# Performance work log

Measured on AMD Instinct MI355X. Metric: run time of the kernel, lower is better.

The kernel has to match this reference:

```python
import jax, jax.numpy as jnp
import numpy as np

N, E, H = 1024, 2048, 32
DIMS = [4, 128, 512, 1028]
NEG_SLOPE_ATT = 0.2   # GATv2 attention LeakyReLU
NEG_SLOPE_ACT = 0.01  # torch.nn.LeakyReLU default


def _lin(key, fan_in, fan_out):
    k1, k2 = jax.random.split(key)
    s = 1.0 / np.sqrt(fan_in)
    return (jax.random.uniform(k1, (fan_in, fan_out), jnp.float32, -s, s),
            jax.random.uniform(k2, (fan_out,), jnp.float32, -s, s))


def setup_inputs() -> dict:
    key = jax.random.key(0)
    ks = jax.random.split(key, 32)
    inp = {
        'x': jax.random.normal(ks[0], (N, 4), jnp.float32),
        'edge_index': jax.random.randint(ks[1], (2, E), 0, N, jnp.int64),
    }
    # GATv2 layers: lin_l/lin_r -> heads*out, att [H, C], bias [C]
    ki = 2
    for i in range(3):
        cin, cout = DIMS[i], DIMS[i + 1]
        wl, bl = _lin(ks[ki], cin, H * cout); ki += 1
        wr, br = _lin(ks[ki], cin, H * cout); ki += 1
        att = jax.random.normal(ks[ki], (H, cout), jnp.float32) * 0.05; ki += 1
        bias = jnp.zeros((cout,), jnp.float32)
        j = i + 1
        inp.update({f'w{j}l': wl, f'b{j}l': bl, f'w{j}r': wr, f'b{j}r': br,
                    f'att{j}': att, f'gb{j}': bias})
    # decoder MLP 1028 -> 512 -> 128 -> 2
    for j, (cin, cout) in enumerate([(1028, 512), (512, 128), (128, 2)], 1):
        w, b = _lin(ks[ki], cin, cout); ki += 1
        inp[f'dw{j}'] = w
        inp[f'db{j}'] = b
    return inp


def _gatv2(x, src, dst, wl, bl, wr, br, att, bias, cout):
    # lin_l on source nodes, lin_r on target nodes (PyG GATv2Conv)
    xl = (x @ wl + bl).reshape(-1, H, cout)   # [N, H, C]
    xr = (x @ wr + br).reshape(-1, H, cout)
    e = jax.nn.leaky_relu(xl[src] + xr[dst], NEG_SLOPE_ATT)  # [Etot, H, C]
    score = jnp.einsum('ehc,hc->eh', e, att)                  # [Etot, H]
    smax = jax.ops.segment_max(score, dst, num_segments=N)
    alpha = jnp.exp(score - smax[dst])
    denom = jax.ops.segment_sum(alpha, dst, num_segments=N)
    alpha = alpha / denom[dst]
    out = jax.ops.segment_sum(alpha[:, :, None] * xl[src], dst, num_segments=N)
    return out.mean(axis=1) + bias  # concat=False: average heads


def reference(x, edge_index,
              w1l, b1l, w1r, b1r, att1, gb1,
              w2l, b2l, w2r, b2r, att2, gb2,
              w3l, b3l, w3r, b3r, att3, gb3,
              dw1, db1, dw2, db2, dw3, db3):
    # add self loops (PyG default)
    loop = jnp.arange(N, dtype=edge_index.dtype)
    src = jnp.concatenate([edge_index[0], loop])
    dst = jnp.concatenate([edge_index[1], loop])

    act = lambda z: jax.nn.leaky_relu(z, NEG_SLOPE_ACT)
    z = _gatv2(x, src, dst, w1l, b1l, w1r, b1r, att1, gb1, 128)
    z = act(z)
    z = _gatv2(z, src, dst, w2l, b2l, w2r, b2r, att2, gb2, 512)
    z = act(z)
    z = _gatv2(z, src, dst, w3l, b3l, w3r, b3r, att3, gb3, 1028)

    z = act(z @ dw1 + db1)
    z = act(z @ dw2 + db2)
    z = z @ dw3 + db3  # [N, 2]
    return z.reshape(-1)
```

## Files before the change

kernel.cpp:

```cpp
#include <hip/hip_runtime.h>
#include <cstdint>
#include <cstddef>

#define NN 1024
#define EE 2048
#define ETOT 3072
#define HH 32

typedef __bf16 bf16_t;
typedef __attribute__((ext_vector_type(8))) __bf16 bf16x8;
typedef __attribute__((ext_vector_type(4))) __bf16 bf16x4;
typedef __attribute__((ext_vector_type(2))) __bf16 bf16x2;
typedef __attribute__((ext_vector_type(4))) float f32x4;

typedef const __attribute__((address_space(1))) void gvoid_t;
typedef __attribute__((address_space(3))) void lvoid_t;

__device__ __forceinline__ void gll16(const void* g, void* l) {
    __builtin_amdgcn_global_load_lds((gvoid_t*)g, (lvoid_t*)l, 16, 0, 0);
}

__global__ void k_zero_int(int* p, int n) {
    int i = blockIdx.x * 256 + threadIdx.x;
    if (i < n) p[i] = 0;
}

__global__ void k_detect(const int* ei, int* flag) {
    int i = blockIdx.x * 256 + threadIdx.x;
    int idx = 2 * i + 1;
    if (idx < 2 * EE && ei[idx] != 0) atomicOr(flag, 1);
}

__global__ void k_edge_prep(const int* ei, const int* flag, int* srcA, int* dstA, int* cnt) {
    int e = blockIdx.x * 256 + threadIdx.x;
    if (e >= ETOT) return;
    int s, d;
    if (e < EE) {
        if (*flag) { s = ei[e]; d = ei[EE + e]; }
        else       { s = ei[2 * e]; d = ei[2 * (EE + e)]; }
        s &= (NN - 1); d &= (NN - 1);
    } else {
        s = d = e - EE;
    }
    srcA[e] = s; dstA[e] = d;
    atomicAdd(&cnt[d], 1);
}

__global__ void k_scan(const int* cnt, int* off) {
    __shared__ int sh[NN];
    int t = threadIdx.x;
    sh[t] = cnt[t];
    __syncthreads();
    for (int o = 1; o < NN; o <<= 1) {
        int v = (t >= o) ? sh[t - o] : 0;
        __syncthreads();
        sh[t] += v;
        __syncthreads();
    }
    off[t + 1] = sh[t];
    if (t == 0) off[0] = 0;
}

__global__ void k_fill(const int* dstA, const int* off, int* cur, int* csre) {
    int e = blockIdx.x * 256 + threadIdx.x;
    if (e >= ETOT) return;
    int d = dstA[e];
    int p = atomicAdd(&cur[d], 1);
    csre[off[d] + p] = e;
}

__global__ void k_convA(const float* __restrict__ A, bf16_t* __restrict__ Ab,
                        int M, int K, int Kp) {
    int idx = blockIdx.x * 256 + threadIdx.x;
    if (idx >= M * Kp) return;
    int m = idx / Kp, k = idx % Kp;
    Ab[idx] = (k < K) ? (bf16_t)A[(size_t)m * K + k] : (bf16_t)0.f;
}

__global__ void k_convB(const float* __restrict__ B, bf16_t* __restrict__ Bt,
                        int K, int Nsub, int ldb, int Kp) {
    __shared__ float sh[32][33];
    int kt = blockIdx.y * 32, nt = blockIdx.x * 32;
    int tx = threadIdx.x & 31, ty = threadIdx.x >> 5;
#pragma unroll
    for (int i = 0; i < 4; ++i) {
        int k = kt + ty + i * 8, n = nt + tx;
        sh[ty + i * 8][tx] = (k < K && n < Nsub) ? B[(size_t)k * ldb + n] : 0.f;
    }
    __syncthreads();
    int kq = (threadIdx.x & 7) * 4;
    int nl = threadIdx.x >> 3;
    int n = nt + nl;
    if (n < Nsub) {
        bf16x4 v;
        v[0] = (bf16_t)sh[kq][nl];
        v[1] = (bf16_t)sh[kq + 1][nl];
        v[2] = (bf16_t)sh[kq + 2][nl];
        v[3] = (bf16_t)sh[kq + 3][nl];
        *(bf16x4*)(&Bt[(size_t)n * Kp + kt + kq]) = v;
    }
}

__global__ __launch_bounds__(256) void k_gemm_bf16(
        const bf16_t* __restrict__ Ab, const bf16_t* __restrict__ Bt,
        const float* __restrict__ bias, void* __restrict__ Cm,
        int M, int Nsub, int Kp, int act, int obf) {
    __shared__ __align__(16) bf16_t SH[24576];
    int tid = threadIdx.x;
    int wave = tid >> 6, lane = tid & 63;
    int wm = (wave & 1) * 64, wn = (wave >> 1) * 64;
    int l16 = lane & 15, lq = lane >> 4;

    int nx = gridDim.x, ny = gridDim.y;
    int bx = blockIdx.x, by = blockIdx.y;
    int total = nx * ny;
    if ((total & 7) == 0) {
        int j = bx + nx * by;
        int w = (j & 7) * (total >> 3) + (j >> 3);
        bx = w / ny;
        by = w % ny;
    }
    int m0 = by * 128, n0 = bx * 128;

    int u0 = wave * 128 + lane;
    int u1 = u0 + 64;
    int r0 = u0 >> 2, s0 = u0 & 3;
    int r1 = u1 >> 2, s1 = u1 & 3;
    int c0 = ((s0 ^ ((r0 >> 1) & 3)) << 3);
    int c1 = ((s1 ^ ((r1 >> 1) & 3)) << 3);
    const bf16_t* gA0 = Ab + (size_t)(m0 + r0) * Kp + c0;
    const bf16_t* gA1 = Ab + (size_t)(m0 + r1) * Kp + c1;
    const bf16_t* gB0 = Bt + (size_t)(n0 + r0) * Kp + c0;
    const bf16_t* gB1 = Bt + (size_t)(n0 + r1) * Kp + c1;

    int cR = ((lq ^ ((l16 >> 1) & 3)) << 3);

    f32x4 acc[4][4] = {};
    int nt = Kp >> 5;

#pragma unroll
    for (int pt = 0; pt < 2; ++pt) {
        bf16_t* d = SH + pt * 8192 + wave * 1024;
        gll16(gA0, d); gll16(gA1, d + 512);
        gll16(gB0, d + 4096); gll16(gB1, d + 4096 + 512);
        gA0 += 32; gA1 += 32; gB0 += 32; gB1 += 32;
    }

    int bc = 0, bn = 2;
    for (int t = 0; t < nt; ++t) {
        if (t + 1 < nt)
            asm volatile("s_waitcnt vmcnt(4) lgkmcnt(0)" ::: "memory");
        else
            asm volatile("s_waitcnt vmcnt(0) lgkmcnt(0)" ::: "memory");
        asm volatile("s_barrier" ::: "memory");
        __builtin_amdgcn_sched_barrier(0);
        if (t + 2 < nt) {
            bf16_t* d = SH + bn * 8192 + wave * 1024;
            gll16(gA0, d); gll16(gA1, d + 512);
            gll16(gB0, d + 4096); gll16(gB1, d + 4096 + 512);
            gA0 += 32; gA1 += 32; gB0 += 32; gB1 += 32;
        }
        const bf16_t* rb = SH + bc * 8192;
        bf16x8 af[4], bfr[4];
#pragma unroll
        for (int mi = 0; mi < 4; ++mi)
            af[mi] = *(const bf16x8*)(rb + (wm + mi * 16 + l16) * 32 + cR);
#pragma unroll
        for (int ni = 0; ni < 4; ++ni)
            bfr[ni] = *(const bf16x8*)(rb + 4096 + (wn + ni * 16 + l16) * 32 + cR);
#pragma unroll
        for (int mi = 0; mi < 4; ++mi)
#pragma unroll
            for (int ni = 0; ni < 4; ++ni)
                acc[mi][ni] = __builtin_amdgcn_mfma_f32_16x16x32_bf16(
                    af[mi], bfr[ni], acc[mi][ni], 0, 0, 0);
        bc = (bc == 2) ? 0 : bc + 1;
        bn = (bn == 2) ? 0 : bn + 1;
    }
    asm volatile("s_waitcnt lgkmcnt(0)" ::: "memory");
    asm volatile("s_barrier" ::: "memory");
    __builtin_amdgcn_sched_barrier(0);

    if (obf) {
#pragma unroll
        for (int ni = 0; ni < 4; ++ni) {
            int cl = wn + ni * 16 + l16;
            float bv = bias[n0 + cl];
#pragma unroll
            for (int mi = 0; mi < 4; ++mi)
#pragma unroll
                for (int r = 0; r < 4; ++r) {
                    int rl = wm + mi * 16 + lq * 4 + r;
                    float v = acc[mi][ni][r] + bv;
                    if (act && v < 0.f) v *= 0.01f;
                    int slot = ((cl >> 3) ^ (rl & 7)) & 15;
                    SH[rl * 128 + slot * 8 + (cl & 7)] = (bf16_t)v;
                }
        }
        __syncthreads();
        bf16_t* Cb = (bf16_t*)Cm;
#pragma unroll
        for (int i = 0; i < 8; ++i) {
            int j = i * 2048 + tid * 8;
            int rl = j >> 7;
            int p = (j >> 3) & 15;
            int cl = ((p ^ (rl & 7)) & 15) * 8;
            bf16x8 v = *(const bf16x8*)(SH + rl * 128 + p * 8);
            int row = m0 + rl, col = n0 + cl;
            if (row < M) {
                if (col + 7 < Nsub) {
                    *(bf16x8*)(Cb + (size_t)row * Nsub + col) = v;
                } else {
#pragma unroll
                    for (int e = 0; e < 8; ++e)
                        if (col + e < Nsub) Cb[(size_t)row * Nsub + col + e] = v[e];
                }
            }
        }
    } else {
#pragma unroll
        for (int ni = 0; ni < 4; ++ni) {
            int col = n0 + wn + ni * 16 + l16;
            if (col >= Nsub) continue;
            float bv = bias[col];
#pragma unroll
            for (int mi = 0; mi < 4; ++mi)
#pragma unroll
                for (int r = 0; r < 4; ++r) {
                    int row = m0 + wm + mi * 16 + lq * 4 + r;
                    if (row < M) {
                        float v = acc[mi][ni][r] + bv;
                        if (act && v < 0.f) v *= 0.01f;
                        ((float*)Cm)[(size_t)row * Nsub + col] = v;
                    }
                }
        }
    }
}

#define TM 64
#define TN 64
#define TK 16
__global__ __launch_bounds__(256) void k_gemm(
        const float* __restrict__ A, const float* __restrict__ B,
        const float* __restrict__ bias, void* __restrict__ Cm,
        int M, int Nsub, int K, int ldb, int act, int obf) {
    __shared__ float As[TK][TM];
    __shared__ float Bs[TK][TN];
    int tid = threadIdx.x;
    int tx = tid % 16, ty = tid / 16;
    int m0 = blockIdx.y * TM, n0 = blockIdx.x * TN;
    float acc[4][4] = {};
    for (int k0 = 0; k0 < K; k0 += TK) {
#pragma unroll
        for (int i = 0; i < 4; ++i) {
            int idx = tid * 4 + i;
            int m = idx >> 4, k = idx & 15;
            float v = 0.f;
            if (k0 + k < K && m0 + m < M) v = A[(size_t)(m0 + m) * K + k0 + k];
            As[k][m] = v;
        }
#pragma unroll
        for (int i = 0; i < 4; ++i) {
            int idx = tid * 4 + i;
            int k = idx >> 6, n = idx & 63;
            float v = 0.f;
            if (k0 + k < K && n0 + n < Nsub) v = B[(size_t)(k0 + k) * ldb + n0 + n];
            Bs[k][n] = v;
        }
        __syncthreads();
#pragma unroll
        for (int kk = 0; kk < TK; ++kk) {
            float4 a4 = *(const float4*)&As[kk][ty * 4];
            float4 b4 = *(const float4*)&Bs[kk][tx * 4];
            float af[4] = {a4.x, a4.y, a4.z, a4.w};
            float bf[4] = {b4.x, b4.y, b4.z, b4.w};
#pragma unroll
            for (int i = 0; i < 4; ++i)
#pragma unroll
                for (int j = 0; j < 4; ++j)
                    acc[i][j] += af[i] * bf[j];
        }
        __syncthreads();
    }
#pragma unroll
    for (int i = 0; i < 4; ++i) {
        int m = m0 + ty * 4 + i;
        if (m >= M) continue;
#pragma unroll
        for (int j = 0; j < 4; ++j) {
            int n = n0 + tx * 4 + j;
            if (n < Nsub) {
                float v = acc[i][j] + bias[n];
                if (act && v < 0.f) v *= 0.01f;
                if (obf) ((bf16_t*)Cm)[(size_t)m * Nsub + n] = (bf16_t)v;
                else     ((float*)Cm)[(size_t)m * Nsub + n] = v;
            }
        }
    }
}

__global__ void k_gemm_naive(const float* __restrict__ A, const float* __restrict__ B,
                             const float* __restrict__ bias, float* __restrict__ out,
                             int M, int N, int K, int act) {
    int idx = blockIdx.x * 256 + threadIdx.x;
    if (idx >= M * N) return;
    int m = idx / N, n = idx % N;
    float s = bias[n];
    for (int k = 0; k < K; ++k)
        s += A[(size_t)m * K + k] * B[(size_t)k * N + n];
    if (act && s < 0.f) s *= 0.01f;
    out[idx] = s;
}

__global__ void k_score(const bf16_t* __restrict__ xl, const bf16_t* __restrict__ xr,
                        const float* __restrict__ att, const int* __restrict__ srcA,
                        const int* __restrict__ dstA, float* __restrict__ sc,
                        int C, int HG, int h0) {
    int wid = (blockIdx.x * 256 + threadIdx.x) >> 6;
    int lane = threadIdx.x & 63;
    if (wid >= ETOT * HG) return;
    int e = wid / HG, hl = wid % HG;
    int s = srcA[e], d = dstA[e];
    const bf16x4* pl = (const bf16x4*)(xl + ((size_t)s * HG + hl) * C);
    const bf16x4* pr = (const bf16x4*)(xr + ((size_t)d * HG + hl) * C);
    const float4* pa = (const float4*)(att + (size_t)(h0 + hl) * C);
    float acc = 0.f;
    int C4 = C >> 2;
    for (int c = lane; c < C4; c += 64) {
        bf16x4 a = pl[c], b = pr[c];
        float4 w = pa[c];
        float v;
        v = (float)a[0] + (float)b[0]; v = v > 0.f ? v : 0.2f * v; acc += v * w.x;
        v = (float)a[1] + (float)b[1]; v = v > 0.f ? v : 0.2f * v; acc += v * w.y;
        v = (float)a[2] + (float)b[2]; v = v > 0.f ? v : 0.2f * v; acc += v * w.z;
        v = (float)a[3] + (float)b[3]; v = v > 0.f ? v : 0.2f * v; acc += v * w.w;
    }
#pragma unroll
    for (int off = 32; off; off >>= 1) acc += __shfl_down(acc, off, 64);
    if (lane == 0) sc[(size_t)e * HH + h0 + hl] = acc;
}

__global__ void k_softmax(const int* __restrict__ off, const int* __restrict__ csre,
                          float* __restrict__ sc, int HG, int h0) {
    int idx = blockIdx.x * 256 + threadIdx.x;
    if (idx >= NN * HG) return;
    int d = idx / HG, h = h0 + idx % HG;
    int b = off[d], en = off[d + 1];
    float m = -1e30f;
    for (int i = b; i < en; ++i) m = fmaxf(m, sc[(size_t)csre[i] * HH + h]);
    float ssum = 0.f;
    for (int i = b; i < en; ++i) ssum += expf(sc[(size_t)csre[i] * HH + h] - m);
    float inv = 1.f / ssum;
    for (int i = b; i < en; ++i) {
        size_t p = (size_t)csre[i] * HH + h;
        sc[p] = expf(sc[p] - m) * inv;
    }
}

__global__ __launch_bounds__(256) void k_aggregate(
        const bf16_t* __restrict__ xl, const float* __restrict__ sc,
        const int* __restrict__ off, const int* __restrict__ csre,
        const int* __restrict__ srcA, const float* __restrict__ bias,
        float* __restrict__ z, int C, int HG, int h0, int lgNC,
        int first, int last, int act) {
    __shared__ float4 sh[256];
    int d = blockIdx.x;
    int NC = 1 << lgNC;
    int c4i = threadIdx.x & (NC - 1);
    int hl = threadIdx.x >> lgNC;
    int c4 = blockIdx.y * NC + c4i;
    int C4 = C >> 2;
    bool active = (c4 < C4);
    float4 acc = {0.f, 0.f, 0.f, 0.f};
    int b = off[d], en = off[d + 1];
    for (int i = b; i < en; ++i) {
        int e = csre[i];
        int s = srcA[e];
        float w = sc[(size_t)e * HH + h0 + hl];
        if (active) {
            bf16x4 vx = *((const bf16x4*)(xl + ((size_t)s * HG + hl) * C) + c4);
            acc.x += w * (float)vx[0];
            acc.y += w * (float)vx[1];
            acc.z += w * (float)vx[2];
            acc.w += w * (float)vx[3];
        }
    }
    sh[threadIdx.x] = acc;
    __syncthreads();
    for (int s = HG >> 1; s >= 1; s >>= 1) {
        if (hl < s) {
            float4 o = sh[threadIdx.x + (s << lgNC)];
            float4 m = sh[threadIdx.x];
            m.x += o.x; m.y += o.y; m.z += o.z; m.w += o.w;
            sh[threadIdx.x] = m;
        }
        __syncthreads();
    }
    if (hl == 0 && active) {
        acc = sh[threadIdx.x];
        float4* zp = (float4*)(z + (size_t)d * C) + c4;
        if (!first) {
            float4 prev = *zp;
            acc.x += prev.x; acc.y += prev.y; acc.z += prev.z; acc.w += prev.w;
        }
        if (last) {
            const float4 bz = *((const float4*)bias + c4);
            acc.x = acc.x * (1.f / 32.f) + bz.x;
            acc.y = acc.y * (1.f / 32.f) + bz.y;
            acc.z = acc.z * (1.f / 32.f) + bz.z;
            acc.w = acc.w * (1.f / 32.f) + bz.w;
            if (act) {
                acc.x = acc.x < 0.f ? acc.x * 0.01f : acc.x;
                acc.y = acc.y < 0.f ? acc.y * 0.01f : acc.y;
                acc.z = acc.z < 0.f ? acc.z * 0.01f : acc.z;
                acc.w = acc.w < 0.f ? acc.w * 0.01f : acc.w;
            }
        }
        *zp = acc;
    }
}

extern "C" void kernel_launch(void* const* d_in, const int* in_sizes, int n_in,
                              void* d_out, int out_size, void* d_ws, size_t ws_size,
                              hipStream_t stream) {
    const float* x   = (const float*)d_in[0];
    const int* ei    = (const int*)d_in[1];
    const float* w1l = (const float*)d_in[2];  const float* b1l = (const float*)d_in[3];
    const float* w1r = (const float*)d_in[4];  const float* b1r = (const float*)d_in[5];
    const float* att1= (const float*)d_in[6];  const float* gb1 = (const float*)d_in[7];
    const float* w2l = (const float*)d_in[8];  const float* b2l = (const float*)d_in[9];
    const float* w2r = (const float*)d_in[10]; const float* b2r = (const float*)d_in[11];
    const float* att2= (const float*)d_in[12]; const float* gb2 = (const float*)d_in[13];
    const float* w3l = (const float*)d_in[14]; const float* b3l = (const float*)d_in[15];
    const float* w3r = (const float*)d_in[16]; const float* b3r = (const float*)d_in[17];
    const float* att3= (const float*)d_in[18]; const float* gb3 = (const float*)d_in[19];
    const float* dw1 = (const float*)d_in[20]; const float* db1 = (const float*)d_in[21];
    const float* dw2 = (const float*)d_in[22]; const float* db2 = (const float*)d_in[23];
    const float* dw3 = (const float*)d_in[24]; const float* db3 = (const float*)d_in[25];
    float* outp = (float*)d_out;

    char* p = (char*)d_ws;
    auto alloc = [&](size_t bytes) -> char* {
        char* r = p;
        p += (bytes + 255) & ~(size_t)255;
        return r;
    };
    float* sc   = (float*)alloc((size_t)ETOT * HH * 4);
    float* za   = (float*)alloc((size_t)NN * 1028 * 4);
    float* zb   = (float*)alloc((size_t)NN * 1028 * 4);
    bf16_t* Abf = (bf16_t*)alloc((size_t)NN * 1056 * 2);
    int*   ints = (int*)  alloc((size_t)(2 * NN + 16) * 4);
    int* cnt  = ints;
    int* cur  = ints + NN;
    int* flag = ints + 2 * NN;
    int* offp = (int*)alloc((size_t)(NN + 1) * 4);
    int* csre = (int*)alloc((size_t)ETOT * 4);
    int* srcA = (int*)alloc((size_t)ETOT * 4);
    int* dstA = (int*)alloc((size_t)ETOT * 4);
    size_t used = (size_t)(p - (char*)d_ws);
    size_t remain = (ws_size > used) ? (ws_size - used) : 0;
    char* chunk = p;

    k_zero_int<<<dim3((2 * NN + 16 + 255) / 256), dim3(256), 0, stream>>>(ints, 2 * NN + 16);
    k_detect<<<dim3((EE + 255) / 256), dim3(256), 0, stream>>>(ei, flag);
    k_edge_prep<<<dim3((ETOT + 255) / 256), dim3(256), 0, stream>>>(ei, flag, srcA, dstA, cnt);
    k_scan<<<dim3(1), dim3(NN), 0, stream>>>(cnt, offp);
    k_fill<<<dim3((ETOT + 255) / 256), dim3(256), 0, stream>>>(dstA, offp, cur, csre);

    struct Layer {
        const float* in; int cin; int C;
        const float *wl, *bl, *wr, *br, *att, *gb;
        float* zout; int act;
    };
    Layer L[3] = {
        { x,    4, 128,  w1l, b1l, w1r, b1r, att1, gb1, za, 1 },
        { za, 128, 512,  w2l, b2l, w2r, b2r, att2, gb2, zb, 1 },
        { zb, 512, 1028, w3l, b3l, w3r, b3r, att3, gb3, za, 0 },
    };
    auto al = [](size_t n) { return (n + 127) & ~(size_t)127; };

    for (int li = 0; li < 3; ++li) {
        int C = L[li].C, K = L[li].cin;
        bool mfma = (K >= 128);
        int Kp = (K + 31) & ~31;
        size_t perHG = 2ull * NN * C * 2 + (mfma ? (size_t)C * Kp * 2 : 0);
        int HG = 32;
        while (HG > 1 && (size_t)HG * perHG + (1u << 20) > remain) HG >>= 1;
        int nchunk = HH / HG;
        int lgNC = 0;
        while ((1 << lgNC) * HG < 256) ++lgNC;
        int NC = 1 << lgNC;
        bf16_t* xlc = (bf16_t*)chunk;
        bf16_t* xrc = xlc + al((size_t)NN * HG * C);
        bf16_t* Bt  = xrc + al((size_t)NN * HG * C);

        if (mfma)
            k_convA<<<dim3((NN * Kp + 255) / 256), dim3(256), 0, stream>>>(L[li].in, Abf, NN, K, Kp);

        for (int hg = 0; hg < nchunk; ++hg) {
            int h0 = hg * HG;
            int colOff = h0 * C;
            int Nsub = HG * C;
            if (mfma) {
                dim3 gc((Nsub + 31) / 32, Kp / 32);
                dim3 gg((Nsub + 127) / 128, NN / 128);
                k_convB<<<gc, dim3(256), 0, stream>>>(L[li].wl + colOff, Bt, K, Nsub, HH * C, Kp);
                k_gemm_bf16<<<gg, dim3(256), 0, stream>>>(Abf, Bt, L[li].bl + colOff, xlc, NN, Nsub, Kp, 0, 1);
                k_convB<<<gc, dim3(256), 0, stream>>>(L[li].wr + colOff, Bt, K, Nsub, HH * C, Kp);
                k_gemm_bf16<<<gg, dim3(256), 0, stream>>>(Abf, Bt, L[li].br + colOff, xrc, NN, Nsub, Kp, 0, 1);
            } else {
                dim3 gg((Nsub + TN - 1) / TN, (NN + TM - 1) / TM);
                k_gemm<<<gg, dim3(256), 0, stream>>>(L[li].in, L[li].wl + colOff, L[li].bl + colOff,
                                                     xlc, NN, Nsub, K, HH * C, 0, 1);
                k_gemm<<<gg, dim3(256), 0, stream>>>(L[li].in, L[li].wr + colOff, L[li].br + colOff,
                                                     xrc, NN, Nsub, K, HH * C, 0, 1);
            }
            int waves = ETOT * HG;
            k_score<<<dim3((waves * 64 + 255) / 256), dim3(256), 0, stream>>>(
                xlc, xrc, L[li].att, srcA, dstA, sc, C, HG, h0);
            k_softmax<<<dim3((NN * HG + 255) / 256), dim3(256), 0, stream>>>(offp, csre, sc, HG, h0);
            int C4 = C >> 2;
            dim3 ga(NN, (C4 + NC - 1) / NC);
            k_aggregate<<<ga, dim3(256), 0, stream>>>(xlc, sc, offp, csre, srcA, L[li].gb,
                                                      L[li].zout, C, HG, h0, lgNC,
                                                      hg == 0, hg == nchunk - 1, L[li].act);
        }
    }

    {
        bf16_t* Bt1  = (bf16_t*)chunk;
        bf16_t* AbD2 = Bt1 + al((size_t)512 * 1056);
        bf16_t* Bt2  = AbD2 + al((size_t)NN * 512);

        k_convA<<<dim3((NN * 1056 + 255) / 256), dim3(256), 0, stream>>>(za, Abf, NN, 1028, 1056);
        k_convB<<<dim3(512 / 32, 1056 / 32), dim3(256), 0, stream>>>(dw1, Bt1, 1028, 512, 512, 1056);
        k_gemm_bf16<<<dim3(512 / 128, NN / 128), dim3(256), 0, stream>>>(Abf, Bt1, db1, AbD2, NN, 512, 1056, 1, 1);

        k_convB<<<dim3(128 / 32, 512 / 32), dim3(256), 0, stream>>>(dw2, Bt2, 512, 128, 128, 512);
        k_gemm_bf16<<<dim3(128 / 128, NN / 128), dim3(256), 0, stream>>>(AbD2, Bt2, db2, za, NN, 128, 512, 1, 0);
    }
    k_gemm_naive<<<dim3((NN * 2 + 255) / 256), dim3(256), 0, stream>>>(za, dw3, db3, outp, NN, 2, 128, 0);
}
```

Baseline: 679.9 us.

## Switch bf16 GEMM to BK=64 double-buffered LDS pipeline

Restructures the MFMA GEMM main loop from a triple-buffered K-step of 32 to a double-buffered K-step of 64, with a new XOR swizzle over 8 chunks per row. The aim is to halve the number of barriers and wait points per unit of K and to issue more MFMAs per synchronization. K padding moves to multiples of 64, so the padded buffers grow, more zero work is done, and LDS use rises to 64 KB per block, which can lower occupancy. Prefetch depth also drops from two tiles ahead to one, which exposes more load latency.

```diff
diff --git a/kernel.cpp b/kernel.cpp
--- a/kernel.cpp
+++ b/kernel.cpp
@@ -105,7 +105,7 @@
         const bf16_t* __restrict__ Ab, const bf16_t* __restrict__ Bt,
         const float* __restrict__ bias, void* __restrict__ Cm,
         int M, int Nsub, int Kp, int act, int obf) {
-    __shared__ __align__(16) bf16_t SH[24576];
+    __shared__ __align__(16) bf16_t SH[32768];
     int tid = threadIdx.x;
     int wave = tid >> 6, lane = tid & 63;
     int wm = (wave & 1) * 64, wn = (wave >> 1) * 64;
@@ -122,64 +122,70 @@
     }
     int m0 = by * 128, n0 = bx * 128;
 
-    int u0 = wave * 128 + lane;
-    int u1 = u0 + 64;
-    int r0 = u0 >> 2, s0 = u0 & 3;
-    int r1 = u1 >> 2, s1 = u1 & 3;
-    int c0 = ((s0 ^ ((r0 >> 1) & 3)) << 3);
-    int c1 = ((s1 ^ ((r1 >> 1) & 3)) << 3);
-    const bf16_t* gA0 = Ab + (size_t)(m0 + r0) * Kp + c0;
-    const bf16_t* gA1 = Ab + (size_t)(m0 + r1) * Kp + c1;
-    const bf16_t* gB0 = Bt + (size_t)(n0 + r0) * Kp + c0;
-    const bf16_t* gB1 = Bt + (size_t)(n0 + r1) * Kp + c1;
-
-    int cR = ((lq ^ ((l16 >> 1) & 3)) << 3);
+    const bf16_t* gA[4];
+    const bf16_t* gB[4];
+#pragma unroll
+    for (int i = 0; i < 4; ++i) {
+        int u = wave * 64 + lane + i * 256;
+        int r = u >> 3, s = u & 7;
+        int c = ((s ^ (r & 7)) << 3);
+        gA[i] = Ab + (size_t)(m0 + r) * Kp + c;
+        gB[i] = Bt + (size_t)(n0 + r) * Kp + c;
+    }
 
     f32x4 acc[4][4] = {};
-    int nt = Kp >> 5;
-
-#pragma unroll
-    for (int pt = 0; pt < 2; ++pt) {
-        bf16_t* d = SH + pt * 8192 + wave * 1024;
-        gll16(gA0, d); gll16(gA1, d + 512);
-        gll16(gB0, d + 4096); gll16(gB1, d + 4096 + 512);
-        gA0 += 32; gA1 += 32; gB0 += 32; gB1 += 32;
-    }
-
-    int bc = 0, bn = 2;
+    int nt = Kp >> 6;
+
+    {
+        bf16_t* dA = SH + wave * 512;
+#pragma unroll
+        for (int i = 0; i < 4; ++i) {
+            gll16(gA[i], dA + i * 2048);
+            gll16(gB[i], dA + 8192 + i * 2048);
+            gA[i] += 64; gB[i] += 64;
+        }
+    }
+    asm volatile("s_waitcnt vmcnt(0)" ::: "memory");
+    asm volatile("s_barrier" ::: "memory");
+    __builtin_amdgcn_sched_barrier(0);
+
+    int bc = 0;
     for (int t = 0; t < nt; ++t) {
-        if (t + 1 < nt)
-            asm volatile("s_waitcnt vmcnt(4) lgkmcnt(0)" ::: "memory");
-        else
-            asm volatile("s_waitcnt vmcnt(0) lgkmcnt(0)" ::: "memory");
+        if (t + 1 < nt) {
+            bf16_t* dA = SH + (bc ^ 1) * 16384 + wave * 512;
+#pragma unroll
+            for (int i = 0; i < 4; ++i) {
+                gll16(gA[i], dA + i * 2048);
+                gll16(gB[i], dA + 8192 + i * 2048);
+                gA[i] += 64; gB[i] += 64;
+            }
+        }
+        __builtin_amdgcn_sched_barrier(0);
+        const bf16_t* rb = SH + bc * 16384;
+        bf16x8 af[2][4], bfr[2][4];
+#pragma unroll
+        for (int kk = 0; kk < 2; ++kk) {
+            int cs = (((kk * 4 + lq) ^ (l16 & 7)) << 3);
+#pragma unroll
+            for (int mi = 0; mi < 4; ++mi)
+                af[kk][mi] = *(const bf16x8*)(rb + (wm + mi * 16 + l16) * 64 + cs);
+#pragma unroll
+            for (int ni = 0; ni < 4; ++ni)
+                bfr[kk][ni] = *(const bf16x8*)(rb + 8192 + (wn + ni * 16 + l16) * 64 + cs);
+        }
+#pragma unroll
+        for (int kk = 0; kk < 2; ++kk)
+#pragma unroll
+            for (int mi = 0; mi < 4; ++mi)
+#pragma unroll
+                for (int ni = 0; ni < 4; ++ni)
+                    acc[mi][ni] = __builtin_amdgcn_mfma_f32_16x16x32_bf16(
+                        af[kk][mi], bfr[kk][ni], acc[mi][ni], 0, 0, 0);
+        asm volatile("s_waitcnt vmcnt(0) lgkmcnt(0)" ::: "memory");
         asm volatile("s_barrier" ::: "memory");
         __builtin_amdgcn_sched_barrier(0);
-        if (t + 2 < nt) {
-            bf16_t* d = SH + bn * 8192 + wave * 1024;
-            gll16(gA0, d); gll16(gA1, d + 512);
-            gll16(gB0, d + 4096); gll16(gB1, d + 4096 + 512);
-            gA0 += 32; gA1 += 32; gB0 += 32; gB1 += 32;
-        }
-        const bf16_t* rb = SH + bc * 8192;
-        bf16x8 af[4], bfr[4];
-#pragma unroll
-        for (int mi = 0; mi < 4; ++mi)
-            af[mi] = *(const bf16x8*)(rb + (wm + mi * 16 + l16) * 32 + cR);
-#pragma unroll
-        for (int ni = 0; ni < 4; ++ni)
-            bfr[ni] = *(const bf16x8*)(rb + 4096 + (wn + ni * 16 + l16) * 32 + cR);
-#pragma unroll
-        for (int mi = 0; mi < 4; ++mi)
-#pragma unroll
-            for (int ni = 0; ni < 4; ++ni)
-                acc[mi][ni] = __builtin_amdgcn_mfma_f32_16x16x32_bf16(
-                    af[mi], bfr[ni], acc[mi][ni], 0, 0, 0);
-        bc = (bc == 2) ? 0 : bc + 1;
-        bn = (bn == 2) ? 0 : bn + 1;
-    }
-    asm volatile("s_waitcnt lgkmcnt(0)" ::: "memory");
-    asm volatile("s_barrier" ::: "memory");
-    __builtin_amdgcn_sched_barrier(0);
+        bc ^= 1;
+    }
 
     if (obf) {
 #pragma unroll
@@ -449,7 +455,7 @@
     float* sc   = (float*)alloc((size_t)ETOT * HH * 4);
     float* za   = (float*)alloc((size_t)NN * 1028 * 4);
     float* zb   = (float*)alloc((size_t)NN * 1028 * 4);
-    bf16_t* Abf = (bf16_t*)alloc((size_t)NN * 1056 * 2);
+    bf16_t* Abf = (bf16_t*)alloc((size_t)NN * 1088 * 2);
     int*   ints = (int*)  alloc((size_t)(2 * NN + 16) * 4);
     int* cnt  = ints;
     int* cur  = ints + NN;
@@ -483,7 +489,7 @@
     for (int li = 0; li < 3; ++li) {
         int C = L[li].C, K = L[li].cin;
         bool mfma = (K >= 128);
-        int Kp = (K + 31) & ~31;
+        int Kp = (K + 63) & ~63;
         size_t perHG = 2ull * NN * C * 2 + (mfma ? (size_t)C * Kp * 2 : 0);
         int HG = 32;
         while (HG > 1 && (size_t)HG * perHG + (1u << 20) > remain) HG >>= 1;
@@ -530,12 +536,12 @@
 
     {
         bf16_t* Bt1  = (bf16_t*)chunk;
-        bf16_t* AbD2 = Bt1 + al((size_t)512 * 1056);
+        bf16_t* AbD2 = Bt1 + al((size_t)512 * 1088);
         bf16_t* Bt2  = AbD2 + al((size_t)NN * 512);
 
-        k_convA<<<dim3((NN * 1056 + 255) / 256), dim3(256), 0, stream>>>(za, Abf, NN, 1028, 1056);
-        k_convB<<<dim3(512 / 32, 1056 / 32), dim3(256), 0, stream>>>(dw1, Bt1, 1028, 512, 512, 1056);
-        k_gemm_bf16<<<dim3(512 / 128, NN / 128), dim3(256), 0, stream>>>(Abf, Bt1, db1, AbD2, NN, 512, 1056, 1, 1);
+        k_convA<<<dim3((NN * 1088 + 255) / 256), dim3(256), 0, stream>>>(za, Abf, NN, 1028, 1088);
+        k_convB<<<dim3(512 / 32, 1088 / 32), dim3(256), 0, stream>>>(dw1, Bt1, 1028, 512, 512, 1088);
+        k_gemm_bf16<<<dim3(512 / 128, NN / 128), dim3(256), 0, stream>>>(Abf, Bt1, db1, AbD2, NN, 512, 1088, 1, 1);
 
         k_convB<<<dim3(128 / 32, 512 / 32), dim3(256), 0, stream>>>(dw2, Bt2, 512, 128, 128, 512);
         k_gemm_bf16<<<dim3(128 / 128, NN / 128), dim3(256), 0, stream>>>(AbD2, Bt2, db2, za, NN, 128, 512, 1, 0);
```

After: 678.2 us. Within noise of the previous version (-0.3%).
